# Optimization experiments

Hardware: AMD Instinct MI355X
Metric: run time of the kernel (lower is better)

## Reference

```python
import jax, jax.numpy as jnp
import numpy as np

B, N, D, H = 4, 2048, 64, 8

def setup_inputs() -> dict:
    key = jax.random.key(0)
    ks = jax.random.split(key, 6)
    s = 0.05
    return {
        "x":  jax.random.normal(ks[0], (B, N, D), dtype=jnp.float32),
        "Wq": jax.random.normal(ks[1], (D, D * H), dtype=jnp.float32) * s,
        "Wk": jax.random.normal(ks[2], (D, D * H), dtype=jnp.float32) * s,
        "Wv": jax.random.normal(ks[3], (D, D * H), dtype=jnp.float32) * s,
        "Wu": jax.random.normal(ks[4], (D * H, D), dtype=jnp.float32) * s,
        "bu": jnp.zeros((D,), dtype=jnp.float32),
    }

def reference(x, Wq, Wk, Wv, Wu, bu):
    b, n, d = x.shape
    h = Wq.shape[1] // d
    # projections: each head has full width d (per the original module)
    q = (x @ Wq).reshape(b, n, h, d).transpose(0, 2, 1, 3)  # [b,h,n,d]
    k = (x @ Wk).reshape(b, n, h, d).transpose(0, 2, 1, 3)
    v = (x @ Wv).reshape(b, n, h, d).transpose(0, 2, 1, 3)
    scores = jnp.einsum('bhnd,bhmd->bhnm', q, k) / jnp.sqrt(jnp.float32(d))
    w = jax.nn.softmax(scores, axis=-1)
    y = jnp.einsum('bhnm,bhmd->bhnd', w, v)          # [b,h,n,d]
    y = y.transpose(0, 2, 1, 3).reshape(b, n, h * d)  # [b,n,h*d]
    return y @ Wu + bu
```

## Files before the change

### kernel.cpp

```cpp
#include <hip/hip_runtime.h>
#include <hip/hip_bf16.h>

#define BB 4
#define NN 2048
#define DD 64
#define HH 8
#define DHH 512

typedef __bf16 bf16_t;
typedef __bf16 bf16x8 __attribute__((ext_vector_type(8)));
typedef __bf16 bf16x4 __attribute__((ext_vector_type(4)));
typedef float f32x4 __attribute__((ext_vector_type(4)));
typedef long long i64;
typedef i64 i64x2 __attribute__((ext_vector_type(2)));
typedef _Float16 f16_t;
typedef _Float16 f16x4 __attribute__((ext_vector_type(4)));
typedef __fp16 h16x2 __attribute__((ext_vector_type(2)));

__device__ __forceinline__ void dma16(const void* g, void* l) {
    __builtin_amdgcn_global_load_lds(
        (const __attribute__((address_space(1))) unsigned int*)g,
        (__attribute__((address_space(3))) unsigned int*)l,
        16, 0, 0);
}

#define MFMA   __builtin_amdgcn_mfma_f32_16x16x32_bf16
#define MFMA8  __builtin_amdgcn_mfma_f32_16x16x32_fp8_fp8
#define MFMA16F __builtin_amdgcn_mfma_f32_16x16x16f16

#define QSCALE 0.18033688011112042f


__global__ __launch_bounds__(256) void prep(
    const float* __restrict__ Wq, const float* __restrict__ Wk,
    const float* __restrict__ Wv, const float* __restrict__ Wu,
    const float* __restrict__ x,
    bf16_t* __restrict__ Wqt, bf16_t* __restrict__ Wkt,
    bf16_t* __restrict__ Wvt, bf16_t* __restrict__ Wut,
    bf16_t* __restrict__ xb)
{
    const int bid = blockIdx.x, tid = threadIdx.x;
    if (bid < 48) {
        const int m = bid >> 4, slice = bid & 15;
        const float* src = (m == 0) ? Wq : (m == 1) ? Wk : Wv;
        bf16_t* dst = (m == 0) ? Wqt : (m == 1) ? Wkt : Wvt;
        const float scale = (m == 0) ? QSCALE : 1.0f;
        const int dc = slice * 32 + (tid >> 3);
        const int kbase = (tid & 7) * 8;
        bf16x8 p;
        #pragma unroll
        for (int j = 0; j < 8; ++j)
            p[j] = (bf16_t)(src[(size_t)(kbase + j) * 512 + dc] * scale);
        *(bf16x8*)(dst + dc * 64 + kbase) = p;
    } else if (bid < 64) {
        const int kq = (bid - 48) * 32;
        const int dc = tid >> 2, sub = (tid & 3) * 8;
        bf16x8 p;
        #pragma unroll
        for (int j = 0; j < 8; ++j)
            p[j] = (bf16_t)Wu[(size_t)(kq + sub + j) * 64 + dc];
        *(bf16x8*)(Wut + dc * 512 + kq + sub) = p;
    } else {
        const int row = (bid - 64) * 256 + tid;
        const float* src = x + (size_t)row * 64;
        bf16_t* dst = xb + (size_t)row * 64;
        #pragma unroll
        for (int g = 0; g < 8; ++g) {
            f32x4 a = *(const f32x4*)(src + g * 8);
            f32x4 b = *(const f32x4*)(src + g * 8 + 4);
            bf16x8 p;
            p[0] = (bf16_t)a[0]; p[1] = (bf16_t)a[1];
            p[2] = (bf16_t)a[2]; p[3] = (bf16_t)a[3];
            p[4] = (bf16_t)b[0]; p[5] = (bf16_t)b[1];
            p[6] = (bf16_t)b[2]; p[7] = (bf16_t)b[3];
            *(bf16x8*)(dst + g * 8) = p;
        }
    }
}

__global__ __launch_bounds__(256) void qkv_mfma(
    const bf16_t* __restrict__ xb, const bf16_t* __restrict__ Wqt,
    const bf16_t* __restrict__ Wkt, const bf16_t* __restrict__ Wvt,
    char* __restrict__ q8, char* __restrict__ k8, f16_t* __restrict__ vt)
{
    const int n0   = blockIdx.x * 64;
    const int h    = blockIdx.y;
    const int tid  = threadIdx.x;
    const int w    = tid >> 6;
    const int lane = tid & 63;
    const int quad = lane >> 4;
    const int c    = lane & 15;
    const int cq   = c & 7;
    const int l8   = lane >> 3;
    const int lg   = (lane & 7) ^ l8;
    const int lo   = l8 * 128 + lg * 16;
    const int sw0  = ((quad    ) ^ cq) * 16;
    const int sw1  = ((quad + 4) ^ cq) * 16;
    const int w2048 = w * 2048;

    __shared__ __align__(16) bf16_t xs2[64 * 64];
    __shared__ __align__(16) bf16_t Wqs[64 * 64], Wks[64 * 64], Wvs[64 * 64];
    __shared__ __align__(16) int qst[64 * 16], kst[64 * 16];

    {
        const char* xg = (const char*)xb + (size_t)n0 * 128;
        dma16(xg + w2048 + lo,        (char*)xs2 + w2048);
        dma16(xg + w2048 + 1024 + lo, (char*)xs2 + w2048 + 1024);
    }
    const char* qg = (const char*)Wqt + (size_t)h * 8192;
    const char* kg = (const char*)Wkt + (size_t)h * 8192;
    const char* vg = (const char*)Wvt + (size_t)h * 8192;
    dma16(qg + w2048 + lo,        (char*)Wqs + w2048);
    dma16(qg + w2048 + 1024 + lo, (char*)Wqs + w2048 + 1024);
    dma16(kg + w2048 + lo,        (char*)Wks + w2048);
    dma16(kg + w2048 + 1024 + lo, (char*)Wks + w2048 + 1024);
    dma16(vg + w2048 + lo,        (char*)Wvs + w2048);
    dma16(vg + w2048 + 1024 + lo, (char*)Wvs + w2048 + 1024);
    __syncthreads();

    auto xfrag2 = [&](int row, int kk) -> bf16x8 {
        return *(const bf16x8*)((const char*)xs2 + row * 128
                                + (((kk * 4 + quad) ^ (row & 7)) * 16));
    };

    bf16x8 xf0 = xfrag2(w * 16 + c, 0);
    bf16x8 xf1 = xfrag2(w * 16 + c, 1);

    const int gr = n0 + w * 16 + c;
    const int nn = gr & 2047;
    const int nsw = (nn & 3) ^ ((nn >> 2) & 3);

    #pragma unroll
    for (int mb = 0; mb < 4; ++mb) {
        const char* aq = (const char*)Wqs + (mb * 16 + c) * 128;
        const char* ak = (const char*)Wks + (mb * 16 + c) * 128;
        f32x4 accq = (f32x4){0.f, 0.f, 0.f, 0.f};
        f32x4 acck = (f32x4){0.f, 0.f, 0.f, 0.f};
        accq = MFMA(*(const bf16x8*)(aq + sw0), xf0, accq, 0, 0, 0);
        accq = MFMA(*(const bf16x8*)(aq + sw1), xf1, accq, 0, 0, 0);
        acck = MFMA(*(const bf16x8*)(ak + sw0), xf0, acck, 0, 0, 0);
        acck = MFMA(*(const bf16x8*)(ak + sw1), xf1, acck, 0, 0, 0);
        int g2  = (mb * 2 + (quad >> 1)) & 3;
        int idx = (quad & 1) + ((mb >> 1) << 1) + ((g2 ^ nsw) << 2);
        int pq = __builtin_amdgcn_cvt_pk_fp8_f32(accq[0], accq[1], 0, false);
        pq     = __builtin_amdgcn_cvt_pk_fp8_f32(accq[2], accq[3], pq, true);
        int pk = __builtin_amdgcn_cvt_pk_fp8_f32(acck[0], acck[1], 0, false);
        pk     = __builtin_amdgcn_cvt_pk_fp8_f32(acck[2], acck[3], pk, true);
        qst[(w * 16 + c) * 16 + idx] = pq;
        kst[(w * 16 + c) * 16 + idx] = pk;
    }

    const char* wvrow = (const char*)Wvs + (w * 16 + c) * 128;
    bf16x8 vf0 = *(const bf16x8*)(wvrow + sw0);
    bf16x8 vf1 = *(const bf16x8*)(wvrow + sw1);

    const int bb2 = n0 >> 11;
    f16_t* vtb = vt + ((size_t)bb2 * HH + h) * (size_t)(DD * NN)
               + (size_t)((n0 & 2047) >> 4) * 1024 + quad * 256 + (w * 16 + c) * 4;

    #pragma unroll
    for (int nb = 0; nb < 4; ++nb) {
        f32x4 acc = (f32x4){0.f, 0.f, 0.f, 0.f};
        acc = MFMA(xfrag2(nb * 16 + c, 0), vf0, acc, 0, 0, 0);
        acc = MFMA(xfrag2(nb * 16 + c, 1), vf1, acc, 0, 0, 0);
        f16x4 p = { (f16_t)acc[0], (f16_t)acc[1], (f16_t)acc[2], (f16_t)acc[3] };
        *(f16x4*)(vtb + nb * 1024) = p;
    }

    {
        const int rl = w * 16 + (lane >> 2);
        const int ch = lane & 3;
        const int grow = n0 + rl;
        const int bb3 = grow >> 11, nn3 = grow & 2047;
        const size_t rowoff = (((size_t)bb3 * HH + h) * NN + nn3) * 64 + ch * 16;
        i64x2 qv = *(const i64x2*)((const char*)qst + rl * 64 + ch * 16);
        i64x2 kv = *(const i64x2*)((const char*)kst + rl * 64 + ch * 16);
        *(i64x2*)(q8 + rowoff) = qv;
        *(i64x2*)(k8 + rowoff) = kv;
    }
}

__global__ __launch_bounds__(256, 3) void flash_attn(
    const char* __restrict__ q8, const char* __restrict__ k8,
    const f16_t* __restrict__ vt, bf16_t* __restrict__ y)
{
    const int h    = blockIdx.x;
    const int n0   = blockIdx.y * 64;
    const int b    = blockIdx.z;
    const int tid  = threadIdx.x;
    const int w    = tid >> 6;
    const int lane = tid & 63;
    const int quad = lane >> 4;
    const int c    = lane & 15;
    const int ksw  = (quad ^ (c & 3) ^ ((c >> 2) & 3)) * 16;

    __shared__ __align__(16) char SM[49152];

    const size_t bh = (size_t)(b * HH + h);
    const char* qp = q8 + bh * (size_t)(NN * 64);
    const char* kp = k8 + bh * (size_t)(NN * 64);
    const char* vp = (const char*)(vt + bh * (size_t)(DD * NN));

    i64x2 qf[4];
    #pragma unroll
    for (int cb = 0; cb < 4; ++cb)
        qf[cb] = *(const i64x2*)(qp + (size_t)(n0 + cb * 16 + c) * 64 + ksw);

    const char* kdma = kp + w * 1024 + lane * 16;
    const char* vdma = vp + w * 2048 + lane * 16;

    const int kro = w * 2048 + c * 64 + ksw;
    const int vro = 8192 + w * 4096 + quad * 512 + c * 8;

    f32x4 lsum4[4];
    f32x4 o[4][4];
    #pragma unroll
    for (int cb = 0; cb < 4; ++cb) lsum4[cb] = (f32x4){0.f, 0.f, 0.f, 0.f};
    #pragma unroll
    for (int db = 0; db < 4; ++db)
        #pragma unroll
        for (int cb = 0; cb < 4; ++cb) o[db][cb] = (f32x4){0.f, 0.f, 0.f, 0.f};

    #define STAGE2(p, buf) do {                                               \
        char* B_ = SM + (buf) * 24576;                                        \
        const size_t t0_ = (size_t)(2 * (p));                                 \
        dma16(kdma + t0_ * 4096,         B_ + w * 2048);                      \
        dma16(kdma + t0_ * 4096 + 4096,  B_ + w * 2048 + 1024);               \
        dma16(vdma + t0_ * 8192,         B_ + 8192 + w * 4096);               \
        dma16(vdma + t0_ * 8192 + 1024,  B_ + 8192 + w * 4096 + 1024);        \
        dma16(vdma + t0_ * 8192 + 8192,  B_ + 8192 + w * 4096 + 2048);        \
        dma16(vdma + t0_ * 8192 + 9216,  B_ + 8192 + w * 4096 + 3072);        \
    } while (0)

    #define BODY2(buf, hf) do {                                               \
        const char* kb_b = SM + (buf) * 24576;                                \
        i64x2 kf_ = *(const i64x2*)(kb_b + kro + (hf) * 1024);                \
        f16x4 vf_[4];                                                         \
        _Pragma("unroll")                                                     \
        for (int db = 0; db < 4; ++db)                                        \
            vf_[db] = *(const f16x4*)(kb_b + vro + (hf) * 2048 + db * 128);   \
        _Pragma("unroll")                                                     \
        for (int cb = 0; cb < 4; ++cb) {                                      \
            f32x4 s_ = (f32x4){0.f, 0.f, 0.f, 0.f};                           \
            s_ = MFMA8(kf_.x, qf[cb].x, s_, 0, 0, 0);                         \
            s_ = MFMA8(kf_.y, qf[cb].y, s_, 0, 0, 0);                         \
            float p0_ = __builtin_amdgcn_exp2f(s_[0]);                        \
            float p1_ = __builtin_amdgcn_exp2f(s_[1]);                        \
            float p2_ = __builtin_amdgcn_exp2f(s_[2]);                        \
            float p3_ = __builtin_amdgcn_exp2f(s_[3]);                        \
            lsum4[cb] += (f32x4){p0_, p1_, p2_, p3_};                         \
            h16x2 ab_ = __builtin_amdgcn_cvt_pkrtz(p0_, p1_);                 \
            h16x2 cd_ = __builtin_amdgcn_cvt_pkrtz(p2_, p3_);                 \
            f16x4 pf_;                                                        \
            __builtin_memcpy(&pf_, &ab_, 4);                                  \
            __builtin_memcpy((char*)&pf_ + 4, &cd_, 4);                       \
            _Pragma("unroll")                                                 \
            for (int db = 0; db < 4; ++db)                                    \
                o[db][cb] = MFMA16F(vf_[db], pf_, o[db][cb], 0, 0, 0);        \
        }                                                                     \
    } while (0)

    STAGE2(0, 0);
    asm volatile("s_waitcnt vmcnt(0)" ::: "memory");
    __builtin_amdgcn_sched_barrier(0);
    STAGE2(1, 1);

    #pragma unroll 1
    for (int p = 0; p < 16; ++p) {
        BODY2(p & 1, 0);
        BODY2(p & 1, 1);
        if (p < 15) {
            __builtin_amdgcn_sched_barrier(0);
            if (p < 14) {
                STAGE2(p + 2, p & 1);
                asm volatile("s_waitcnt vmcnt(6)" ::: "memory");
            } else {
                asm volatile("s_waitcnt vmcnt(0)" ::: "memory");
            }
            __builtin_amdgcn_sched_barrier(0);
        }
    }

    #undef STAGE2
    #undef BODY2

    float lsum[4];
    #pragma unroll
    for (int cb = 0; cb < 4; ++cb)
        lsum[cb] = (lsum4[cb][0] + lsum4[cb][1]) + (lsum4[cb][2] + lsum4[cb][3]);

    __syncthreads();

    char*  Ob = SM;
    float* Lb = (float*)(SM + 16384);

    #pragma unroll
    for (int cb = 0; cb < 4; ++cb) {
        lsum[cb] += __shfl_xor(lsum[cb], 16, 64);
        lsum[cb] += __shfl_xor(lsum[cb], 32, 64);
    }
    if (quad == 0) {
        #pragma unroll
        for (int cb = 0; cb < 4; ++cb)
            Lb[(w * 4 + cb) * 16 + c] = lsum[cb];
    }

    #pragma unroll
    for (int ww = 0; ww < 4; ++ww) {
        if (w == ww) {
            #pragma unroll
            for (int db = 0; db < 4; ++db) {
                #pragma unroll
                for (int cb = 0; cb < 4; ++cb) {
                    char* p = Ob + (size_t)(((db * 4 + cb) * 4 + quad) * 16 + c) * 16;
                    f32x4 v = o[db][cb];
                    if (ww > 0) v += *(const f32x4*)p;
                    *(f32x4*)p = v;
                }
            }
        }
        __syncthreads();
    }

    {
        const int n_loc = tid & 63;
        const int dq    = tid >> 6;
        const int qcb   = n_loc >> 4;
        const int cc    = n_loc & 15;
        float l = Lb[(0 * 4 + qcb) * 16 + cc] + Lb[(1 * 4 + qcb) * 16 + cc]
                + Lb[(2 * 4 + qcb) * 16 + cc] + Lb[(3 * 4 + qcb) * 16 + cc];
        float inv = 1.0f / l;
        float vals[16];
        #pragma unroll
        for (int q2 = 0; q2 < 4; ++q2) {
            f32x4 v = *(const f32x4*)(Ob
                    + (size_t)(((dq * 4 + qcb) * 4 + q2) * 16 + cc) * 16);
            vals[q2 * 4 + 0] = v[0]; vals[q2 * 4 + 1] = v[1];
            vals[q2 * 4 + 2] = v[2]; vals[q2 * 4 + 3] = v[3];
        }
        bf16x8 o0, o1;
        #pragma unroll
        for (int j = 0; j < 8; ++j) {
            o0[j] = (bf16_t)(vals[j] * inv);
            o1[j] = (bf16_t)(vals[8 + j] * inv);
        }
        bf16_t* yrow = y + bh * (size_t)(NN * DD) + (size_t)(n0 + n_loc) * DD + dq * 16;
        *(bf16x8*)(yrow)     = o0;
        *(bf16x8*)(yrow + 8) = o1;
    }
}

__global__ __launch_bounds__(256) void out_proj(
    const bf16_t* __restrict__ y,
    const bf16_t* __restrict__ Wut,
    const float* __restrict__ bu, float* __restrict__ out)
{
    const int rt   = blockIdx.x >> 1;
    const int dh   = blockIdx.x & 1;
    const int row0 = rt * 32;
    const int b    = row0 >> 11;
    const int nn0  = row0 & 2047;
    const int tid  = threadIdx.x;
    const int w    = tid >> 6;
    const int lane = tid & 63;
    const int quad = lane >> 4;
    const int c    = lane & 15;
    const int cq   = c & 7;

    __shared__ __align__(16) bf16_t ys[32 * 512];

    {
        const int hsel = lane >> 3;
        const int g7   = lane & 7;
        #pragma unroll
        for (int rr = 0; rr < 8; ++rr) {
            int row = w * 8 + rr;
            const char* src = (const char*)y
                + (((size_t)b * HH + hsel) * NN + nn0 + row) * 128
                + ((g7 ^ (row & 7)) * 16);
            dma16(src, (char*)ys + row * 1024);
        }
    }
    __syncthreads();

    const int rows16 = (w >> 1) * 16;
    const int mb     = dh * 2 + (w & 1);
    const char* yrow = (const char*)ys + (rows16 + c) * 1024;

    f32x4 acc = (f32x4){0.f, 0.f, 0.f, 0.f};
    #pragma unroll
    for (int kk = 0; kk < 16; ++kk) {
        int g = kk * 4 + quad;
        bf16x8 bfrag = *(const bf16x8*)(yrow + (((g & ~7) | ((g & 7) ^ cq)) * 16));
        bf16x8 afrag = *(const bf16x8*)((const char*)Wut
                        + (size_t)(mb * 16 + c) * 1024 + kk * 64 + quad * 16);
        acc = MFMA(afrag, bfrag, acc, 0, 0, 0);
    }

    float4 bb = *(const float4*)(bu + mb * 16 + quad * 4);
    float4 res = { acc[0] + bb.x, acc[1] + bb.y, acc[2] + bb.z, acc[3] + bb.w };
    float* op = out + (size_t)(row0 + rows16 + c) * DD + mb * 16 + quad * 4;
    *(float4*)op = res;
}

extern "C" void kernel_launch(void* const* d_in, const int* in_sizes, int n_in,
                              void* d_out, int out_size, void* d_ws, size_t ws_size,
                              hipStream_t stream) {
    const float* x  = (const float*)d_in[0];
    const float* Wq = (const float*)d_in[1];
    const float* Wk = (const float*)d_in[2];
    const float* Wv = (const float*)d_in[3];
    const float* Wu = (const float*)d_in[4];
    const float* bu = (const float*)d_in[5];
    float* out = (float*)d_out;

    const size_t SEG8 = (size_t)BB * HH * NN * 64;
    const size_t SEG  = SEG8 * 2;
    char* ws = (char*)d_ws;
    char*   q8  = ws;
    char*   k8  = ws + SEG8;
    f16_t*  vt  = (f16_t*)(ws + 2 * SEG8);
    bf16_t* y   = (bf16_t*)(ws + 2 * SEG8 + SEG);
    bf16_t* Wqt = (bf16_t*)(ws + 2 * SEG8 + 2 * SEG);
    bf16_t* Wkt = (bf16_t*)(ws + 2 * SEG8 + 2 * SEG + (1 << 16));
    bf16_t* Wvt = (bf16_t*)(ws + 2 * SEG8 + 2 * SEG + 2 * (1 << 16));
    bf16_t* Wut = (bf16_t*)(ws + 2 * SEG8 + 2 * SEG + 3 * (1 << 16));
    bf16_t* xb  = (bf16_t*)(ws + 2 * SEG8 + 2 * SEG + 4 * (1 << 16));

    prep<<<dim3(96), dim3(256), 0, stream>>>(Wq, Wk, Wv, Wu, x,
                                             Wqt, Wkt, Wvt, Wut, xb);
    qkv_mfma<<<dim3(128, 8), dim3(256), 0, stream>>>(xb, Wqt, Wkt, Wvt, q8, k8, vt);
    flash_attn<<<dim3(HH, NN / 64, BB), dim3(256), 0, stream>>>(q8, k8, vt, y);
    out_proj<<<dim3(512), dim3(256), 0, stream>>>(y, Wut, bu, out);
}
```

Measured before the change: 126.7 us.

## Read QKV weight fragments from global directly and split attention launch in two

The QKV projection kernel stops staging the Wq/Wk/Wv head slices in LDS through async DMA. It now loads the MFMA weight fragments straight from global memory, which cuts LDS use and removes the DMA for the weights. Separately, the flash attention launch is split into two launches of two batches each, using a new z offset argument. This may change tail and wave scheduling, but it adds one more launch overhead.

After: 137.4 us. +8.4%, slower.

```diff
diff --git a/kernel.cpp b/kernel.cpp
--- a/kernel.cpp
+++ b/kernel.cpp
@@ -9,7 +9,6 @@
 
 typedef __bf16 bf16_t;
 typedef __bf16 bf16x8 __attribute__((ext_vector_type(8)));
-typedef __bf16 bf16x4 __attribute__((ext_vector_type(4)));
 typedef float f32x4 __attribute__((ext_vector_type(4)));
 typedef long long i64;
 typedef i64 i64x2 __attribute__((ext_vector_type(2)));
@@ -90,16 +89,12 @@
     const int lane = tid & 63;
     const int quad = lane >> 4;
     const int c    = lane & 15;
-    const int cq   = c & 7;
     const int l8   = lane >> 3;
     const int lg   = (lane & 7) ^ l8;
     const int lo   = l8 * 128 + lg * 16;
-    const int sw0  = ((quad    ) ^ cq) * 16;
-    const int sw1  = ((quad + 4) ^ cq) * 16;
     const int w2048 = w * 2048;
 
     __shared__ __align__(16) bf16_t xs2[64 * 64];
-    __shared__ __align__(16) bf16_t Wqs[64 * 64], Wks[64 * 64], Wvs[64 * 64];
     __shared__ __align__(16) int qst[64 * 16], kst[64 * 16];
 
     {
@@ -107,15 +102,6 @@
         dma16(xg + w2048 + lo,        (char*)xs2 + w2048);
         dma16(xg + w2048 + 1024 + lo, (char*)xs2 + w2048 + 1024);
     }
-    const char* qg = (const char*)Wqt + (size_t)h * 8192;
-    const char* kg = (const char*)Wkt + (size_t)h * 8192;
-    const char* vg = (const char*)Wvt + (size_t)h * 8192;
-    dma16(qg + w2048 + lo,        (char*)Wqs + w2048);
-    dma16(qg + w2048 + 1024 + lo, (char*)Wqs + w2048 + 1024);
-    dma16(kg + w2048 + lo,        (char*)Wks + w2048);
-    dma16(kg + w2048 + 1024 + lo, (char*)Wks + w2048 + 1024);
-    dma16(vg + w2048 + lo,        (char*)Wvs + w2048);
-    dma16(vg + w2048 + 1024 + lo, (char*)Wvs + w2048 + 1024);
     __syncthreads();
 
     auto xfrag2 = [&](int row, int kk) -> bf16x8 {
@@ -126,20 +112,24 @@
     bf16x8 xf0 = xfrag2(w * 16 + c, 0);
     bf16x8 xf1 = xfrag2(w * 16 + c, 1);
 
+    const char* wqb = (const char*)Wqt + (size_t)h * 8192;
+    const char* wkb = (const char*)Wkt + (size_t)h * 8192;
+    const char* wvb = (const char*)Wvt + (size_t)h * 8192;
+
     const int gr = n0 + w * 16 + c;
     const int nn = gr & 2047;
     const int nsw = (nn & 3) ^ ((nn >> 2) & 3);
 
     #pragma unroll
     for (int mb = 0; mb < 4; ++mb) {
-        const char* aq = (const char*)Wqs + (mb * 16 + c) * 128;
-        const char* ak = (const char*)Wks + (mb * 16 + c) * 128;
+        const char* qr = wqb + (size_t)(mb * 16 + c) * 128;
+        const char* kr = wkb + (size_t)(mb * 16 + c) * 128;
         f32x4 accq = (f32x4){0.f, 0.f, 0.f, 0.f};
         f32x4 acck = (f32x4){0.f, 0.f, 0.f, 0.f};
-        accq = MFMA(*(const bf16x8*)(aq + sw0), xf0, accq, 0, 0, 0);
-        accq = MFMA(*(const bf16x8*)(aq + sw1), xf1, accq, 0, 0, 0);
-        acck = MFMA(*(const bf16x8*)(ak + sw0), xf0, acck, 0, 0, 0);
-        acck = MFMA(*(const bf16x8*)(ak + sw1), xf1, acck, 0, 0, 0);
+        accq = MFMA(*(const bf16x8*)(qr + quad * 16),      xf0, accq, 0, 0, 0);
+        accq = MFMA(*(const bf16x8*)(qr + 64 + quad * 16), xf1, accq, 0, 0, 0);
+        acck = MFMA(*(const bf16x8*)(kr + quad * 16),      xf0, acck, 0, 0, 0);
+        acck = MFMA(*(const bf16x8*)(kr + 64 + quad * 16), xf1, acck, 0, 0, 0);
         int g2  = (mb * 2 + (quad >> 1)) & 3;
         int idx = (quad & 1) + ((mb >> 1) << 1) + ((g2 ^ nsw) << 2);
         int pq = __builtin_amdgcn_cvt_pk_fp8_f32(accq[0], accq[1], 0, false);
@@ -150,9 +140,9 @@
         kst[(w * 16 + c) * 16 + idx] = pk;
     }
 
-    const char* wvrow = (const char*)Wvs + (w * 16 + c) * 128;
-    bf16x8 vf0 = *(const bf16x8*)(wvrow + sw0);
-    bf16x8 vf1 = *(const bf16x8*)(wvrow + sw1);
+    const char* vr = wvb + (size_t)(w * 16 + c) * 128;
+    bf16x8 vf0 = *(const bf16x8*)(vr + quad * 16);
+    bf16x8 vf1 = *(const bf16x8*)(vr + 64 + quad * 16);
 
     const int bb2 = n0 >> 11;
     f16_t* vtb = vt + ((size_t)bb2 * HH + h) * (size_t)(DD * NN)
@@ -182,11 +172,11 @@
 
 __global__ __launch_bounds__(256, 3) void flash_attn(
     const char* __restrict__ q8, const char* __restrict__ k8,
-    const f16_t* __restrict__ vt, bf16_t* __restrict__ y)
+    const f16_t* __restrict__ vt, bf16_t* __restrict__ y, const int zoff)
 {
     const int h    = blockIdx.x;
     const int n0   = blockIdx.y * 64;
-    const int b    = blockIdx.z;
+    const int b    = blockIdx.z + zoff;
     const int tid  = threadIdx.x;
     const int w    = tid >> 6;
     const int lane = tid & 63;
@@ -430,6 +420,7 @@
     prep<<<dim3(96), dim3(256), 0, stream>>>(Wq, Wk, Wv, Wu, x,
                                              Wqt, Wkt, Wvt, Wut, xb);
     qkv_mfma<<<dim3(128, 8), dim3(256), 0, stream>>>(xb, Wqt, Wkt, Wvt, q8, k8, vt);
-    flash_attn<<<dim3(HH, NN / 64, BB), dim3(256), 0, stream>>>(q8, k8, vt, y);
+    flash_attn<<<dim3(HH, NN / 64, 2), dim3(256), 0, stream>>>(q8, k8, vt, y, 0);
+    flash_attn<<<dim3(HH, NN / 64, 2), dim3(256), 0, stream>>>(q8, k8, vt, y, 2);
     out_proj<<<dim3(512), dim3(256), 0, stream>>>(y, Wut, bu, out);
 }
```
